# Performance work log

Hardware: AMD Instinct MI355X
Metric: run time of the kernel (lower is better)

Reference implementation:

```python
import jax, jax.numpy as jnp
import numpy as np

N_ATOMS = 1_000_000
N_GRAPHS = 8192
FEA_DIM = 64
HIDDEN = 32
N_HEAD = 3


def setup_inputs() -> dict:
    key = jax.random.key(0)
    k1, k2, k3, k4, k5, k6 = jax.random.split(key, 6)
    atom_feas = jax.random.normal(k1, (N_ATOMS, FEA_DIM), dtype=jnp.float32)
    atom_owner = jnp.sort(jax.random.randint(k2, (N_ATOMS,), 0, N_GRAPHS))
    s1 = 1.0 / np.sqrt(FEA_DIM)
    s2 = 1.0 / np.sqrt(HIDDEN)
    W1 = jax.random.uniform(k3, (FEA_DIM, HIDDEN), jnp.float32, -s1, s1)
    b1 = jax.random.uniform(k4, (HIDDEN,), jnp.float32, -s1, s1)
    W2 = jax.random.uniform(k5, (HIDDEN, N_HEAD), jnp.float32, -s2, s2)
    b2 = jax.random.uniform(k6, (N_HEAD,), jnp.float32, -s2, s2)
    return {"atom_feas": atom_feas, "atom_owner": atom_owner,
            "W1": W1, "b1": b1, "W2": W2, "b2": b2}


def reference(atom_feas, atom_owner, W1, b1, W2, b2):
    # key MLP: Linear -> SiLU -> Linear, producing per-atom, per-head logits [N, H]
    h = jax.nn.silu(atom_feas @ W1 + b1)
    logits = h @ W2 + b2  # [N, H]
    # per-graph (segment) softmax over atoms, independently per head
    seg_max = jax.ops.segment_max(logits, atom_owner, num_segments=N_GRAPHS)  # [G, H]
    e = jnp.exp(logits - seg_max[atom_owner])
    denom = jax.ops.segment_sum(e, atom_owner, num_segments=N_GRAPHS)  # [G, H]
    w = e / denom[atom_owner]  # [N, H]
    # attention-weighted pooling: per graph, atom_fea.T @ w -> [D, H] flattened row-major
    outer = (atom_feas[:, :, None] * w[:, None, :]).reshape(atom_feas.shape[0], FEA_DIM * N_HEAD)
    crystal_feas = jax.ops.segment_sum(outer, atom_owner, num_segments=N_GRAPHS)  # [G, D*H]
    return crystal_feas
```

## Files before the change

kernel.cpp:

```cpp
#include <hip/hip_runtime.h>
#include <math.h>
#include <stdint.h>

#define NFEA   64
#define NHEAD  3

typedef float v2f __attribute__((ext_vector_type(2)));

__global__ void gar_starts(const int* __restrict__ owner, int* __restrict__ starts,
                           int n_atoms, int n_graphs)
{
  int a = blockIdx.x * blockDim.x + threadIdx.x;
  if (a >= n_atoms) return;
  int cur  = owner[a];
  int prev = (a == 0) ? -1 : owner[a - 1];
  for (int g = prev + 1; g <= cur; ++g) starts[g] = a;
  if (a == n_atoms - 1)
    for (int g = cur + 1; g <= n_graphs; ++g) starts[g] = n_atoms;
}

__global__ __launch_bounds__(256, 4) void gar_fused(
    const float* __restrict__ atom_feas,
    const int*   __restrict__ owner,
    const int*   __restrict__ starts,
    const float* __restrict__ W1, const float* __restrict__ b1,
    const float* __restrict__ W2, const float* __restrict__ b2,
    float* __restrict__ out,
    float* __restrict__ denom,
    int n_atoms)
{
  __shared__ __align__(16) float4 e4[256];
  const int tid = threadIdx.x;
  const int blockstart = blockIdx.x * 256;
  const int a = blockstart + tid;
  const bool act = a < n_atoms;
  const int ar = act ? a : n_atoms - 1;

  const float4* __restrict__ xrow = (const float4*)(atom_feas + (size_t)ar * NFEA);
  float4 xr[16];
#pragma unroll
  for (int q = 0; q < 16; ++q) xr[q] = xrow[q];

  v2f h[16];
#pragma unroll
  for (int j = 0; j < 16; ++j) h[j] = ((const v2f*)b1)[j];

#pragma unroll
  for (int q = 0; q < 16; ++q) {
    float xs[4] = {xr[q].x, xr[q].y, xr[q].z, xr[q].w};
#pragma unroll
    for (int dd = 0; dd < 4; ++dd) {
      v2f xd2 = {xs[dd], xs[dd]};
      const v2f* wrow = ((const v2f*)W1) + (q * 4 + dd) * 16;
#pragma unroll
      for (int jj = 0; jj < 16; ++jj)
        h[jj] = __builtin_elementwise_fma(xd2, wrow[jj], h[jj]);
    }
  }
  float l0 = b2[0], l1 = b2[1], l2 = b2[2];
#pragma unroll
  for (int jj = 0; jj < 16; ++jj) {
#pragma unroll
    for (int cc = 0; cc < 2; ++cc) {
      float hj = h[jj][cc];
      float s = hj * __builtin_amdgcn_rcpf(1.0f + __expf(-hj));
      int k = 2 * jj + cc;
      l0 = fmaf(s, W2[k * 3 + 0], l0);
      l1 = fmaf(s, W2[k * 3 + 1], l1);
      l2 = fmaf(s, W2[k * 3 + 2], l2);
    }
  }
  const float e0 = act ? __expf(l0) : 0.f;
  const float e1 = act ? __expf(l1) : 0.f;
  const float e2 = act ? __expf(l2) : 0.f;
  e4[tid] = make_float4(e0, e1, e2, 0.f);
  __syncthreads();

  const int blockend = (blockstart + 256 < n_atoms) ? blockstart + 256 : n_atoms;
  const int g0 = owner[blockstart];
  const int g1 = owner[blockend - 1];
  const int w = tid >> 6, t = tid & 63;

  for (int g = g0; g <= g1; ++g) {
    int lo = starts[g];     if (lo < blockstart) lo = blockstart;
    int hi = starts[g + 1]; if (hi > blockend)   hi = blockend;
    if (lo >= hi) continue;

    float a0 = 0.f, a1 = 0.f, a2 = 0.f;
    float dd0 = 0.f, dd1 = 0.f, dd2 = 0.f;
    for (int i = lo + w; i < hi; i += 4) {
      float4 ev = e4[i - blockstart];
      float xv = atom_feas[(size_t)i * NFEA + t];
      a0 = fmaf(ev.x, xv, a0);
      a1 = fmaf(ev.y, xv, a1);
      a2 = fmaf(ev.z, xv, a2);
      dd0 += ev.x; dd1 += ev.y; dd2 += ev.z;
    }
    float* og = out + (size_t)g * (NFEA * NHEAD) + t * 3;
    atomicAdd(og + 0, a0);
    atomicAdd(og + 1, a1);
    atomicAdd(og + 2, a2);
    if (t == 0) {
      atomicAdd(&denom[g * 3 + 0], dd0);
      atomicAdd(&denom[g * 3 + 1], dd1);
      atomicAdd(&denom[g * 3 + 2], dd2);
    }
  }
}

__global__ void gar_norm(float* __restrict__ out, const float* __restrict__ denom,
                         int total)
{
  int i = blockIdx.x * 256 + threadIdx.x;
  if (i >= total) return;
  int g = i / (NFEA * NHEAD);
  int h = i % NHEAD;
  float dn = denom[g * 3 + h];
  float v = out[i];
  out[i] = dn > 0.f ? v / dn : 0.f;
}

extern "C" void kernel_launch(void* const* d_in, const int* in_sizes, int n_in,
                              void* d_out, int out_size, void* d_ws, size_t ws_size,
                              hipStream_t stream)
{
  const float* atom_feas = (const float*)d_in[0];
  const int*   owner     = (const int*)d_in[1];
  const float* W1        = (const float*)d_in[2];
  const float* b1        = (const float*)d_in[3];
  const float* W2        = (const float*)d_in[4];
  const float* b2        = (const float*)d_in[5];
  float* out = (float*)d_out;

  const int n_atoms  = in_sizes[1];
  const int n_graphs = out_size / (NFEA * NHEAD);

  int* starts = (int*)d_ws;
  const size_t den_off = (((size_t)(n_graphs + 1) * sizeof(int)) + 255) & ~(size_t)255;
  float* denom = (float*)((char*)d_ws + den_off);

  hipMemsetAsync(out, 0, (size_t)out_size * sizeof(float), stream);
  hipMemsetAsync(denom, 0, (size_t)n_graphs * 3 * sizeof(float), stream);

  hipLaunchKernelGGL(gar_starts, dim3((n_atoms + 255) / 256), dim3(256), 0, stream,
                     owner, starts, n_atoms, n_graphs);
  hipLaunchKernelGGL(gar_fused, dim3((n_atoms + 255) / 256), dim3(256), 0, stream,
                     atom_feas, owner, starts, W1, b1, W2, b2, out, denom, n_atoms);
  hipLaunchKernelGGL(gar_norm, dim3((out_size + 255) / 256), dim3(256), 0, stream,
                     out, denom, out_size);
}
```

Measured before the change: 482.4 us.

## Replace global atomics with per-block partial slots and a reduce kernel

Each wave now owns whole graph segments inside the block instead of all four waves striding one graph. Per-graph partial sums are written to slot buffers indexed by the block's offset from the graph's first block, and only overflow slots use atomics. A new reduce kernel sums the slots and applies the softmax denominator, replacing the atomic-heavy epilogue and the separate normalization pass. This adds a larger workspace buffer plus a memset of the atomic slot, changes launch bounds from 4 to 3, and inserts a compiler memory barrier after the row loads.

```diff
diff --git a/kernel.cpp b/kernel.cpp
--- a/kernel.cpp
+++ b/kernel.cpp
@@ -2,8 +2,10 @@
 #include <math.h>
 #include <stdint.h>
 
-#define NFEA   64
-#define NHEAD  3
+#define NFEA    64
+#define NHEAD   3
+#define PSTRIDE 256
+#define KSLOT   4
 
 typedef float v2f __attribute__((ext_vector_type(2)));
 
@@ -19,15 +21,14 @@
     for (int g = cur + 1; g <= n_graphs; ++g) starts[g] = n_atoms;
 }
 
-__global__ __launch_bounds__(256, 4) void gar_fused(
+__global__ __launch_bounds__(256, 3) void gar_fused(
     const float* __restrict__ atom_feas,
     const int*   __restrict__ owner,
     const int*   __restrict__ starts,
     const float* __restrict__ W1, const float* __restrict__ b1,
     const float* __restrict__ W2, const float* __restrict__ b2,
-    float* __restrict__ out,
-    float* __restrict__ denom,
-    int n_atoms)
+    float* __restrict__ partials,
+    int n_atoms, int n_graphs)
 {
   __shared__ __align__(16) float4 e4[256];
   const int tid = threadIdx.x;
@@ -40,6 +41,7 @@
   float4 xr[16];
 #pragma unroll
   for (int q = 0; q < 16; ++q) xr[q] = xrow[q];
+  asm volatile("" ::: "memory");
 
   v2f h[16];
 #pragma unroll
@@ -70,10 +72,9 @@
       l2 = fmaf(s, W2[k * 3 + 2], l2);
     }
   }
-  const float e0 = act ? __expf(l0) : 0.f;
-  const float e1 = act ? __expf(l1) : 0.f;
-  const float e2 = act ? __expf(l2) : 0.f;
-  e4[tid] = make_float4(e0, e1, e2, 0.f);
+  e4[tid] = make_float4(act ? __expf(l0) : 0.f,
+                        act ? __expf(l1) : 0.f,
+                        act ? __expf(l2) : 0.f, 0.f);
   __syncthreads();
 
   const int blockend = (blockstart + 256 < n_atoms) ? blockstart + 256 : n_atoms;
@@ -81,43 +82,63 @@
   const int g1 = owner[blockend - 1];
   const int w = tid >> 6, t = tid & 63;
 
-  for (int g = g0; g <= g1; ++g) {
-    int lo = starts[g];     if (lo < blockstart) lo = blockstart;
+  for (int g = g0 + w; g <= g1; g += 4) {
+    const int gs0 = starts[g];
+    int lo = gs0;           if (lo < blockstart) lo = blockstart;
     int hi = starts[g + 1]; if (hi > blockend)   hi = blockend;
     if (lo >= hi) continue;
 
     float a0 = 0.f, a1 = 0.f, a2 = 0.f;
     float dd0 = 0.f, dd1 = 0.f, dd2 = 0.f;
-    for (int i = lo + w; i < hi; i += 4) {
+    for (int i = lo; i < hi; ++i) {
       float4 ev = e4[i - blockstart];
-      float xv = atom_feas[(size_t)i * NFEA + t];
+      float  xv = atom_feas[(size_t)i * NFEA + t];
       a0 = fmaf(ev.x, xv, a0);
       a1 = fmaf(ev.y, xv, a1);
       a2 = fmaf(ev.z, xv, a2);
       dd0 += ev.x; dd1 += ev.y; dd2 += ev.z;
     }
-    float* og = out + (size_t)g * (NFEA * NHEAD) + t * 3;
-    atomicAdd(og + 0, a0);
-    atomicAdd(og + 1, a1);
-    atomicAdd(og + 2, a2);
-    if (t == 0) {
-      atomicAdd(&denom[g * 3 + 0], dd0);
-      atomicAdd(&denom[g * 3 + 1], dd1);
-      atomicAdd(&denom[g * 3 + 2], dd2);
+    const int slot = blockIdx.x - (gs0 >> 8);
+    if (slot < KSLOT - 1) {
+      float* P = partials + ((size_t)slot * n_graphs + g) * PSTRIDE;
+      P[t * 3 + 0] = a0; P[t * 3 + 1] = a1; P[t * 3 + 2] = a2;
+      if (t == 0) { P[192] = dd0; P[193] = dd1; P[194] = dd2; }
+    } else {
+      float* P = partials + ((size_t)(KSLOT - 1) * n_graphs + g) * PSTRIDE;
+      atomicAdd(P + t * 3 + 0, a0);
+      atomicAdd(P + t * 3 + 1, a1);
+      atomicAdd(P + t * 3 + 2, a2);
+      if (t == 0) { atomicAdd(P + 192, dd0); atomicAdd(P + 193, dd1); atomicAdd(P + 194, dd2); }
     }
   }
 }
 
-__global__ void gar_norm(float* __restrict__ out, const float* __restrict__ denom,
-                         int total)
+__global__ __launch_bounds__(256, 8) void gar_reduce(
+    const int* __restrict__ starts,
+    const float* __restrict__ partials,
+    float* __restrict__ out, int n_graphs)
 {
-  int i = blockIdx.x * 256 + threadIdx.x;
-  if (i >= total) return;
-  int g = i / (NFEA * NHEAD);
-  int h = i % NHEAD;
-  float dn = denom[g * 3 + h];
-  float v = out[i];
-  out[i] = dn > 0.f ? v / dn : 0.f;
+  const int g = blockIdx.x * 4 + (threadIdx.x >> 6);
+  const int t = threadIdx.x & 63;
+  if (g >= n_graphs) return;
+  const int s0 = starts[g], s1 = starts[g + 1];
+
+  const float* P3 = partials + ((size_t)(KSLOT - 1) * n_graphs + g) * PSTRIDE;
+  float n0 = P3[t * 3 + 0], n1 = P3[t * 3 + 1], n2 = P3[t * 3 + 2];
+  float dn0 = P3[192], dn1 = P3[193], dn2 = P3[194];
+
+  int span = 0;
+  if (s1 > s0) span = ((s1 - 1) >> 8) - (s0 >> 8) + 1;
+  const int kmax = span < (KSLOT - 1) ? span : (KSLOT - 1);
+  for (int k = 0; k < kmax; ++k) {
+    const float* P = partials + ((size_t)k * n_graphs + g) * PSTRIDE;
+    n0 += P[t * 3 + 0]; n1 += P[t * 3 + 1]; n2 += P[t * 3 + 2];
+    dn0 += P[192]; dn1 += P[193]; dn2 += P[194];
+  }
+  float* og = out + (size_t)g * (NFEA * NHEAD);
+  og[t * 3 + 0] = dn0 > 0.f ? n0 / dn0 : 0.f;
+  og[t * 3 + 1] = dn1 > 0.f ? n1 / dn1 : 0.f;
+  og[t * 3 + 2] = dn2 > 0.f ? n2 / dn2 : 0.f;
 }
 
 extern "C" void kernel_launch(void* const* d_in, const int* in_sizes, int n_in,
@@ -136,16 +157,17 @@
   const int n_graphs = out_size / (NFEA * NHEAD);
 
   int* starts = (int*)d_ws;
-  const size_t den_off = (((size_t)(n_graphs + 1) * sizeof(int)) + 255) & ~(size_t)255;
-  float* denom = (float*)((char*)d_ws + den_off);
+  const size_t par_off = (((size_t)(n_graphs + 1) * sizeof(int)) + 255) & ~(size_t)255;
+  float* partials = (float*)((char*)d_ws + par_off);
 
-  hipMemsetAsync(out, 0, (size_t)out_size * sizeof(float), stream);
-  hipMemsetAsync(denom, 0, (size_t)n_graphs * 3 * sizeof(float), stream);
+  hipMemsetAsync(partials + (size_t)(KSLOT - 1) * n_graphs * PSTRIDE, 0,
+                 (size_t)n_graphs * PSTRIDE * sizeof(float), stream);
 
   hipLaunchKernelGGL(gar_starts, dim3((n_atoms + 255) / 256), dim3(256), 0, stream,
                      owner, starts, n_atoms, n_graphs);
   hipLaunchKernelGGL(gar_fused, dim3((n_atoms + 255) / 256), dim3(256), 0, stream,
-                     atom_feas, owner, starts, W1, b1, W2, b2, out, denom, n_atoms);
-  hipLaunchKernelGGL(gar_norm, dim3((out_size + 255) / 256), dim3(256), 0, stream,
-                     out, denom, out_size);
+                     atom_feas, owner, starts, W1, b1, W2, b2, partials,
+                     n_atoms, n_graphs);
+  hipLaunchKernelGGL(gar_reduce, dim3((n_graphs + 3) / 4), dim3(256), 0, stream,
+                     starts, partials, out, n_graphs);
 }
```

New measurement: 484.4 us. No clear change (+0.4%).
